# Performance work log

Hardware: AMD Instinct MI355X
Metric: run time of the kernel (lower is better)

## Reference

```python
import jax, jax.numpy as jnp
import numpy as np

NEG_INF = -1e30  # large negative instead of float('-inf') for fp16/bf16 safety in softmax


def setup_inputs() -> dict:
    key = jax.random.key(0)
    k1, k2, k3, k4 = jax.random.split(key, 4)
    B, T, C, H = 8, 2048, 768, 64
    x = jax.random.normal(k1, (B, T, C), dtype=jnp.float32)
    # nn.Linear(n_embd, head_size, bias=False): y = x @ W.T, W shape (head_size, n_embd)
    s = 1.0 / np.sqrt(C)
    Wk = jax.random.uniform(k2, (H, C), dtype=jnp.float32, minval=-s, maxval=s)
    Wq = jax.random.uniform(k3, (H, C), dtype=jnp.float32, minval=-s, maxval=s)
    Wv = jax.random.uniform(k4, (H, C), dtype=jnp.float32, minval=-s, maxval=s)
    return {"x": x, "Wk": Wk, "Wq": Wq, "Wv": Wv}


def reference(x, Wk, Wq, Wv):
    # x: [B,T,C]; Wk/Wq/Wv: [H,C]
    k = jnp.einsum('btc,hc->bth', x, Wk)  # [B,T,H]
    q = jnp.einsum('btc,hc->bth', x, Wq)
    v = jnp.einsum('btc,hc->bth', x, Wv)
    att = jnp.einsum('bqh,bkh->bqk', q, k)  # [B,T,T], NOTE: no 1/sqrt(H) scaling, faithful to source
    T = x.shape[1]
    causal = jnp.tril(jnp.ones((T, T), dtype=bool))
    att = jnp.where(causal, att, NEG_INF)
    att = jax.nn.softmax(att, axis=-1)
    out = jnp.einsum('bqk,bkh->bqh', att, v)  # [B,T,H]
    return out
```

## Files before the change

kernel.cpp:

```cpp
#include <hip/hip_runtime.h>
#include <hip/hip_bf16.h>
#include <stdint.h>

typedef float    f32x4  __attribute__((ext_vector_type(4)));
typedef float    f32x16 __attribute__((ext_vector_type(16)));
typedef short    s16x8  __attribute__((ext_vector_type(8)));
typedef uint32_t u32x4  __attribute__((ext_vector_type(4)));
typedef uint32_t u32x2  __attribute__((ext_vector_type(2)));

#define NB 8
#define NT 2048
#define NC 768
#define NH 64
#define LOG2E 1.4426950408889634f

__device__ __forceinline__ uint32_t f2bf1(float f) {
  union { float f; uint32_t u; } v; v.f = f;
  uint32_t u = v.u;
  return (u + 0x7fffu + ((u >> 16) & 1u)) >> 16;
}
__device__ __forceinline__ uint32_t packbf2(float lo, float hi) {
  union { __hip_bfloat162 h; uint32_t u; } c;
  c.h = __float22bfloat162_rn(float2{lo, hi});
  return c.u;
}
__device__ __forceinline__ float bf2f(short s) {
  union { float f; uint32_t u; } v; v.u = ((uint32_t)(uint16_t)s) << 16; return v.f;
}

__global__ __launch_bounds__(256) void wconv_kernel(
    const float* __restrict__ Wk, const float* __restrict__ Wq,
    const float* __restrict__ Wv, short* __restrict__ Wf)
{
  int f = blockIdx.x * 256 + threadIdx.x;
  int lane = f & 63;
  int rest = f >> 6;
  int ks = rest % 48;
  int nt = rest / 48;
  int col = lane & 31, half = lane >> 5;
  int n = nt * 32 + col;
  int k = ks * 16 + half * 8;
  const float* src;
  float sc = 1.0f;
  if (n < 64)       { src = Wq + (size_t)n * NC + k; sc = LOG2E; }
  else if (n < 128) { src = Wk + (size_t)(n - 64) * NC + k; }
  else              { src = Wv + (size_t)(n - 128) * NC + k; }
  f32x4 a = *(const f32x4*)src;
  f32x4 b = *(const f32x4*)(src + 4);
  u32x4 o = {packbf2(a[0] * sc, a[1] * sc), packbf2(a[2] * sc, a[3] * sc),
             packbf2(b[0] * sc, b[1] * sc), packbf2(b[2] * sc, b[3] * sc)};
  *(u32x4*)&Wf[(size_t)f * 8] = o;
}

__global__ __launch_bounds__(256, 2) void proj_kernel(
    const float* __restrict__ x, const short* __restrict__ Wf,
    short* __restrict__ qf_buf, short* __restrict__ kf_buf, short* __restrict__ vf_buf)
{
  __shared__ char smem[49152];
  short* ldsX  = (short*)smem;
  float* slot0 = (float*)smem;
  float* slot1 = (float*)(smem + 24576);
  short* ldsQT = (short*)(smem + 24576);
  short* ldsKT = ldsQT + 2176;
  short* ldsVT = ldsQT + 4352;

  const int tid  = threadIdx.x;
  const int lane = tid & 63;
  const int w    = tid >> 6;
  const int col  = lane & 31;
  const int half = lane >> 5;
  const int t0   = blockIdx.x * 32;

  {
    const int tok = tid >> 3, g = tid & 7;
    const float* src = x + (size_t)(t0 + tok) * NC + g * 8;
    short* drow = ldsX + tok * 768;
#pragma unroll
    for (int i = 0; i < 12; ++i) {
      f32x4 a = *(const f32x4*)(src + i * 64);
      f32x4 b = *(const f32x4*)(src + i * 64 + 4);
      int grp = g + i * 8;
      int swz = (grp & ~7) | ((grp ^ tok) & 7);
      u32x4 o = {packbf2(a[0], a[1]), packbf2(a[2], a[3]),
                 packbf2(b[0], b[1]), packbf2(b[2], b[3])};
      *(u32x4*)&drow[swz * 8] = o;
    }
  }
  __syncthreads();

  f32x16 acc[6];
#pragma unroll
  for (int j = 0; j < 6; ++j)
#pragma unroll
    for (int e = 0; e < 16; ++e) acc[j][e] = 0.f;

  const short* wbase = Wf + lane * 8;
  auto loadW = [&](s16x8* d, int ks) {
#pragma unroll
    for (int nt = 0; nt < 6; ++nt)
      d[nt] = *(const s16x8*)(wbase + ((size_t)(nt * 48 + ks) << 9));
  };
  auto loadA = [&](int ks) -> s16x8 {
    int grp = ks * 2 + half;
    int swz = (grp & ~7) | ((grp ^ col) & 7);
    return *(const s16x8*)&ldsX[col * 768 + swz * 8];
  };

  {
    const int ks0 = w * 12;
    s16x8 wA[6], wB[6], aA, aB;
    loadW(wA, ks0);
    aA = loadA(ks0);
#pragma unroll
    for (int s = 0; s < 12; s += 2) {
      loadW(wB, ks0 + s + 1);
      aB = loadA(ks0 + s + 1);
#pragma unroll
      for (int nt = 0; nt < 6; ++nt)
        acc[nt] = __builtin_amdgcn_mfma_f32_32x32x16_bf16(aA, wA[nt], acc[nt], 0, 0, 0);
      if (s + 2 < 12) { loadW(wA, ks0 + s + 2); aA = loadA(ks0 + s + 2); }
#pragma unroll
      for (int nt = 0; nt < 6; ++nt)
        acc[nt] = __builtin_amdgcn_mfma_f32_32x32x16_bf16(aB, wB[nt], acc[nt], 0, 0, 0);
    }
  }

  auto putSlot = [&](float* sl) {
#pragma unroll
    for (int nt = 0; nt < 6; ++nt)
#pragma unroll
      for (int r = 0; r < 16; ++r) {
        int rd = (r & 3) + 8 * (r >> 2) + 4 * half;
        sl[rd * 192 + nt * 32 + col] = acc[nt][r];
      }
  };
  auto addSlot = [&](float* sl) {
#pragma unroll
    for (int nt = 0; nt < 6; ++nt)
#pragma unroll
      for (int r = 0; r < 16; ++r) {
        int rd = (r & 3) + 8 * (r >> 2) + 4 * half;
        acc[nt][r] += sl[rd * 192 + nt * 32 + col];
      }
  };

  __syncthreads();
  if (w >= 2) putSlot(w == 2 ? slot0 : slot1);
  __syncthreads();
  if (w < 2) addSlot(w == 0 ? slot0 : slot1);
  __syncthreads();
  if (w == 1) putSlot(slot0);
  __syncthreads();
  if (w == 0) {
    addSlot(slot0);
#pragma unroll
    for (int nt = 0; nt < 6; ++nt) {
      int n = nt * 32 + col;
#pragma unroll
      for (int r = 0; r < 16; ++r) {
        int rd = (r & 3) + 8 * (r >> 2) + 4 * half;
        short v = (short)f2bf1(acc[nt][r]);
        if (n < 64)       ldsQT[rd * 68 + n] = v;
        else if (n < 128) ldsKT[rd * 68 + (n - 64)] = v;
        else              ldsVT[(n - 128) * 34 + rd] = v;
      }
    }
  }
  __syncthreads();

  {
    const int b  = t0 >> 11;
    const int kt = (t0 >> 5) & 63;
    const size_t base = (size_t)(b * 64 + kt) * 2048;
    s16x8 vq = *(const s16x8*)&ldsQT[col * 68 + w * 16 + half * 8];
    *(s16x8*)&qf_buf[base + w * 512 + lane * 8] = vq;
    s16x8 vk = *(const s16x8*)&ldsKT[col * 68 + w * 16 + half * 8];
    *(s16x8*)&kf_buf[base + w * 512 + lane * 8] = vk;
    s16x8 vv = *(const s16x8*)&ldsVT[(col + (w >> 1) * 32) * 34 + (w & 1) * 16 + half * 8];
    *(s16x8*)&vf_buf[base + w * 512 + lane * 8] = vv;
  }
}

__global__ __launch_bounds__(512, 2) void attn_kernel(
    const short* __restrict__ qf_buf, const short* __restrict__ kf_buf,
    const short* __restrict__ vf_buf, float* __restrict__ out)
{
  __shared__ short ldsOb[8][32][72];
  __shared__ float ldsM[8][32];
  __shared__ float ldsL[8][32];

  const int tid  = threadIdx.x;
  const int lane = tid & 63;
  const int w    = tid >> 6;
  const int col  = lane & 31;
  const int half = lane >> 5;
  const int b    = blockIdx.x & 7;
  const int pr   = blockIdx.x >> 3;
  const int qtL = pr, qtH = 63 - pr;
  const int Hn = 64 - pr, Ln = pr + 1;
  int nH = (8 * Hn + 32) / 65;
  if (nH < 1) nH = 1;
  if (nH > 7) nH = 7;
  const int nL = 8 - nH;

  int qt, tBeg, tEnd;
  if (w < nH) { qt = qtH; tBeg = (w * Hn) / nH; tEnd = ((w + 1) * Hn) / nH; }
  else        { int wl = w - nH; qt = qtL; tBeg = (wl * Ln) / nL; tEnd = ((wl + 1) * Ln) / nL; }

  s16x8 qf[4];
  {
    const short* qp = qf_buf + (size_t)(b * 64 + qt) * 2048 + lane * 8;
#pragma unroll
    for (int ks = 0; ks < 4; ++ks) qf[ks] = *(const s16x8*)(qp + ks * 512);
  }
  const short* kfb = kf_buf + (size_t)b * 64 * 2048 + lane * 8;
  const short* vfb = vf_buf + (size_t)b * 64 * 2048 + lane * 8;

  f32x16 oacc[2];
#pragma unroll
  for (int i = 0; i < 2; ++i)
#pragma unroll
    for (int e = 0; e < 16; ++e) oacc[i][e] = 0.f;
  float m = -1e30f, l = 0.f;

  s16x8 kA[4], vA[4], kB[4], vB[4];
  auto loadT = [&](s16x8* dk, s16x8* dv, int t) {
    const short* kp = kfb + (size_t)t * 2048;
    const short* vp = vfb + (size_t)t * 2048;
#pragma unroll
    for (int i = 0; i < 4; ++i) {
      dk[i] = *(const s16x8*)(kp + i * 512);
      dv[i] = *(const s16x8*)(vp + i * 512);
    }
  };
  auto body = [&](s16x8* ck, s16x8* cv, int t) {
    f32x16 s;
#pragma unroll
    for (int e = 0; e < 16; ++e) s[e] = 0.f;
#pragma unroll
    for (int ks = 0; ks < 4; ++ks)
      s = __builtin_amdgcn_mfma_f32_32x32x16_bf16(ck[ks], qf[ks], s, 0, 0, 0);

    if (t == qt) {
#pragma unroll
      for (int r = 0; r < 16; ++r) {
        int rd = (r & 3) + 8 * (r >> 2) + 4 * half;
        if (rd > col) s[r] = -1e30f;
      }
    }
    float vmax = s[0];
#pragma unroll
    for (int r = 1; r < 16; ++r) vmax = fmaxf(vmax, s[r]);
    vmax = fmaxf(vmax, __shfl_xor(vmax, 32));
    float mn    = fmaxf(m, vmax);
    float alpha = exp2f(m - mn);
    float p[16];
    float rs = 0.f;
#pragma unroll
    for (int r = 0; r < 16; ++r) { p[r] = exp2f(s[r] - mn); rs += p[r]; }
    rs += __shfl_xor(rs, 32);
    l = l * alpha + rs;
    m = mn;
#pragma unroll
    for (int i = 0; i < 2; ++i)
#pragma unroll
      for (int e = 0; e < 16; ++e) oacc[i][e] *= alpha;

    uint32_t pw[8];
#pragma unroll
    for (int i = 0; i < 8; ++i) pw[i] = packbf2(p[2 * i], p[2 * i + 1]);
#pragma unroll
    for (int kc = 0; kc < 2; ++kc) {
      uint32_t s0 = half ? pw[4 * kc]     : pw[4 * kc + 2];
      uint32_t s1 = half ? pw[4 * kc + 1] : pw[4 * kc + 3];
      uint32_t r0 = __shfl_xor(s0, 32);
      uint32_t r1 = __shfl_xor(s1, 32);
      uint32_t w0 = half ? r0 : pw[4 * kc];
      uint32_t w1 = half ? r1 : pw[4 * kc + 1];
      uint32_t w2 = half ? pw[4 * kc + 2] : r0;
      uint32_t w3 = half ? pw[4 * kc + 3] : r1;
      union { u32x4 u; s16x8 v; } pf;
      pf.u = (u32x4){w0, w1, w2, w3};
#pragma unroll
      for (int ht = 0; ht < 2; ++ht)
        oacc[ht] = __builtin_amdgcn_mfma_f32_32x32x16_bf16(cv[ht * 2 + kc], pf.v, oacc[ht], 0, 0, 0);
    }
  };

  int t = tBeg;
  if (t < tEnd) loadT(kA, vA, t);
  if (t + 1 < tEnd) loadT(kB, vB, t + 1);
  for (; t + 1 < tEnd; t += 2) {
    body(kA, vA, t);
    if (t + 2 < tEnd) loadT(kA, vA, t + 2);
    body(kB, vB, t + 1);
    if (t + 3 < tEnd) loadT(kB, vB, t + 3);
  }
  if (t < tEnd) body(kA, vA, t);

  if (half == 0) { ldsM[w][col] = m; ldsL[w][col] = l; }
#pragma unroll
  for (int ht = 0; ht < 2; ++ht)
#pragma unroll
    for (int u = 0; u < 4; ++u) {
      int h = ht * 32 + 8 * u + 4 * half;
      u32x2 pk = {packbf2(oacc[ht][4 * u + 0], oacc[ht][4 * u + 1]),
                  packbf2(oacc[ht][4 * u + 2], oacc[ht][4 * u + 3])};
      *(u32x2*)&ldsOb[w][col][h] = pk;
    }
  __syncthreads();

  {
    const int seg = tid >> 8;
    const int rr  = (tid >> 3) & 31;
    const int h0  = (tid & 7) * 8;
    const int s0  = seg ? nH : 0;
    const int s1  = seg ? 8 : nH;
    float M = -1e30f;
    for (int s = s0; s < s1; ++s) M = fmaxf(M, ldsM[s][rr]);
    float Ls = 0.f;
    float o[8];
#pragma unroll
    for (int j = 0; j < 8; ++j) o[j] = 0.f;
    for (int s = s0; s < s1; ++s) {
      float cf = exp2f(ldsM[s][rr] - M);
      Ls += cf * ldsL[s][rr];
      s16x8 raw = *(const s16x8*)&ldsOb[s][rr][h0];
#pragma unroll
      for (int j = 0; j < 8; ++j) o[j] += cf * bf2f(raw[j]);
    }
    float inv = 1.0f / Ls;
    int qrow = (seg ? qtL : qtH) * 32 + rr;
    float* ob = out + (size_t)(b * NT + qrow) * NH + h0;
    *(f32x4*)ob       = (f32x4){o[0] * inv, o[1] * inv, o[2] * inv, o[3] * inv};
    *(f32x4*)(ob + 4) = (f32x4){o[4] * inv, o[5] * inv, o[6] * inv, o[7] * inv};
  }
}

extern "C" void kernel_launch(void* const* d_in, const int* in_sizes, int n_in,
                              void* d_out, int out_size, void* d_ws, size_t ws_size,
                              hipStream_t stream) {
  const float* x  = (const float*)d_in[0];
  const float* Wk = (const float*)d_in[1];
  const float* Wq = (const float*)d_in[2];
  const float* Wv = (const float*)d_in[3];
  float* out = (float*)d_out;

  char* ws = (char*)d_ws;
  short* Wf  = (short*)(ws);
  short* qfb = (short*)(ws + (512 << 10));
  short* kfb = (short*)(ws + (512 << 10) + (2 << 20));
  short* vfb = (short*)(ws + (512 << 10) + (4 << 20));

  hipLaunchKernelGGL(wconv_kernel, dim3(72),  dim3(256), 0, stream, Wk, Wq, Wv, Wf);
  hipLaunchKernelGGL(proj_kernel,  dim3(512), dim3(256), 0, stream, x, Wf, qfb, kfb, vfb);
  hipLaunchKernelGGL(attn_kernel,  dim3(256), dim3(512), 0, stream, qfb, kfb, vfb, out);
}
```

Measured before the change: 115.6 us.

## Fuse projection and attention into one cooperative kernel with grid sync

The projection and attention kernels are merged into a single cooperative launch of 256 blocks of 512 threads. Each block first projects two 32-token tiles, with eight waves splitting K and N four by two, then all blocks meet at a grid-wide barrier before running the attention phase unchanged. This removes one kernel launch and its drain/fill gap. In exchange, the projection phase runs on half as many blocks, the cooperative launch and grid barrier add their own overhead, and correctness depends on all blocks being co-resident.

```diff
diff --git a/kernel.cpp b/kernel.cpp
--- a/kernel.cpp
+++ b/kernel.cpp
@@ -1,6 +1,9 @@
 #include <hip/hip_runtime.h>
 #include <hip/hip_bf16.h>
+#include <hip/hip_cooperative_groups.h>
 #include <stdint.h>
+
+namespace cg = cooperative_groups;
 
 typedef float    f32x4  __attribute__((ext_vector_type(4)));
 typedef float    f32x16 __attribute__((ext_vector_type(16)));
@@ -52,288 +55,294 @@
   *(u32x4*)&Wf[(size_t)f * 8] = o;
 }
 
-__global__ __launch_bounds__(256, 2) void proj_kernel(
+__global__ __launch_bounds__(512, 2) void fused_kernel(
     const float* __restrict__ x, const short* __restrict__ Wf,
-    short* __restrict__ qf_buf, short* __restrict__ kf_buf, short* __restrict__ vf_buf)
+    short* __restrict__ qfb, short* __restrict__ kfb, short* __restrict__ vfb,
+    float* __restrict__ out)
 {
   __shared__ char smem[49152];
-  short* ldsX  = (short*)smem;
-  float* slot0 = (float*)smem;
-  float* slot1 = (float*)(smem + 24576);
-  short* ldsQT = (short*)(smem + 24576);
-  short* ldsKT = ldsQT + 2176;
-  short* ldsVT = ldsQT + 4352;
 
   const int tid  = threadIdx.x;
   const int lane = tid & 63;
-  const int w    = tid >> 6;
+  const int w8   = tid >> 6;
   const int col  = lane & 31;
   const int half = lane >> 5;
-  const int t0   = blockIdx.x * 32;
+  const int blk  = blockIdx.x;
+  const int b    = blk & 7;
+  const int pr   = blk >> 3;
 
   {
-    const int tok = tid >> 3, g = tid & 7;
-    const float* src = x + (size_t)(t0 + tok) * NC + g * 8;
-    short* drow = ldsX + tok * 768;
-#pragma unroll
-    for (int i = 0; i < 12; ++i) {
-      f32x4 a = *(const f32x4*)(src + i * 64);
-      f32x4 b = *(const f32x4*)(src + i * 64 + 4);
-      int grp = g + i * 8;
-      int swz = (grp & ~7) | ((grp ^ tok) & 7);
-      u32x4 o = {packbf2(a[0], a[1]), packbf2(a[2], a[3]),
-                 packbf2(b[0], b[1]), packbf2(b[2], b[3])};
-      *(u32x4*)&drow[swz * 8] = o;
+    short* ldsX = (short*)smem;
+    const int kh = w8 >> 1;
+    const int nh = w8 & 1;
+
+    for (int sub = 0; sub < 2; ++sub) {
+      const int kt = pr * 2 + sub;
+      const int tg = b * 64 + kt;
+      const int t0 = tg * 32;
+
+      {
+        const int tok = tid >> 4, g16 = tid & 15;
+        const float* src = x + (size_t)(t0 + tok) * NC + g16 * 8;
+        short* drow = ldsX + tok * 768;
+#pragma unroll
+        for (int i = 0; i < 6; ++i) {
+          f32x4 a = *(const f32x4*)(src + i * 128);
+          f32x4 c = *(const f32x4*)(src + i * 128 + 4);
+          int grp = g16 + i * 16;
+          int swz = (grp & ~7) | ((grp ^ tok) & 7);
+          u32x4 o = {packbf2(a[0], a[1]), packbf2(a[2], a[3]),
+                     packbf2(c[0], c[1]), packbf2(c[2], c[3])};
+          *(u32x4*)&drow[swz * 8] = o;
+        }
+      }
+      __syncthreads();
+
+      f32x16 acc[3];
+#pragma unroll
+      for (int j = 0; j < 3; ++j)
+#pragma unroll
+        for (int e = 0; e < 16; ++e) acc[j][e] = 0.f;
+
+      const short* wbase = Wf + lane * 8;
+      auto loadW = [&](s16x8* d, int ks) {
+#pragma unroll
+        for (int j = 0; j < 3; ++j)
+          d[j] = *(const s16x8*)(wbase + ((size_t)((nh * 3 + j) * 48 + ks) << 9));
+      };
+      auto loadA = [&](int ks) -> s16x8 {
+        int grp = ks * 2 + half;
+        int swz = (grp & ~7) | ((grp ^ col) & 7);
+        return *(const s16x8*)&ldsX[col * 768 + swz * 8];
+      };
+      {
+        const int ks0 = kh * 12;
+        s16x8 wA[3], wB[3], aA, aB;
+        loadW(wA, ks0); aA = loadA(ks0);
+#pragma unroll
+        for (int s = 0; s < 12; s += 2) {
+          loadW(wB, ks0 + s + 1); aB = loadA(ks0 + s + 1);
+#pragma unroll
+          for (int j = 0; j < 3; ++j)
+            acc[j] = __builtin_amdgcn_mfma_f32_32x32x16_bf16(aA, wA[j], acc[j], 0, 0, 0);
+          if (s + 2 < 12) { loadW(wA, ks0 + s + 2); aA = loadA(ks0 + s + 2); }
+#pragma unroll
+          for (int j = 0; j < 3; ++j)
+            acc[j] = __builtin_amdgcn_mfma_f32_32x32x16_bf16(aB, wB[j], acc[j], 0, 0, 0);
+        }
+      }
+      __syncthreads();
+
+      auto slot = [&](int i) { return (float*)(smem + i * 12288); };
+      auto putSlot = [&](float* sl) {
+#pragma unroll
+        for (int j = 0; j < 3; ++j)
+#pragma unroll
+          for (int r = 0; r < 16; ++r) {
+            int rd = (r & 3) + 8 * (r >> 2) + 4 * half;
+            sl[rd * 96 + j * 32 + col] = acc[j][r];
+          }
+      };
+      auto addSlot = [&](float* sl) {
+#pragma unroll
+        for (int j = 0; j < 3; ++j)
+#pragma unroll
+          for (int r = 0; r < 16; ++r) {
+            int rd = (r & 3) + 8 * (r >> 2) + 4 * half;
+            acc[j][r] += sl[rd * 96 + j * 32 + col];
+          }
+      };
+      if (kh >= 2) putSlot(slot((kh - 2) * 2 + nh));
+      __syncthreads();
+      if (kh == 0) addSlot(slot(nh));
+      if (kh == 1) addSlot(slot(2 + nh));
+      __syncthreads();
+      if (kh == 1) putSlot(slot(nh));
+      __syncthreads();
+
+      short* ldsQT = (short*)(smem + 24576);
+      short* ldsKT = ldsQT + 2176;
+      short* ldsVT = ldsQT + 4352;
+      if (kh == 0) {
+        addSlot(slot(nh));
+#pragma unroll
+        for (int j = 0; j < 3; ++j) {
+          int n = nh * 96 + j * 32 + col;
+#pragma unroll
+          for (int r = 0; r < 16; ++r) {
+            int rd = (r & 3) + 8 * (r >> 2) + 4 * half;
+            short v = (short)f2bf1(acc[j][r]);
+            if (n < 64)       ldsQT[rd * 68 + n] = v;
+            else if (n < 128) ldsKT[rd * 68 + (n - 64)] = v;
+            else              ldsVT[(n - 128) * 34 + rd] = v;
+          }
+        }
+      }
+      __syncthreads();
+
+      {
+        const size_t base = (size_t)tg * 2048;
+        if (w8 < 4) {
+          s16x8 vq = *(const s16x8*)&ldsQT[col * 68 + w8 * 16 + half * 8];
+          *(s16x8*)&qfb[base + w8 * 512 + lane * 8] = vq;
+          s16x8 vk = *(const s16x8*)&ldsKT[col * 68 + w8 * 16 + half * 8];
+          *(s16x8*)&kfb[base + w8 * 512 + lane * 8] = vk;
+        } else {
+          int i = w8 - 4;
+          s16x8 vv = *(const s16x8*)&ldsVT[(col + (i >> 1) * 32) * 34 + (i & 1) * 16 + half * 8];
+          *(s16x8*)&vfb[base + i * 512 + lane * 8] = vv;
+        }
+      }
+      __syncthreads();
     }
   }
-  __syncthreads();
-
-  f32x16 acc[6];
-#pragma unroll
-  for (int j = 0; j < 6; ++j)
-#pragma unroll
-    for (int e = 0; e < 16; ++e) acc[j][e] = 0.f;
-
-  const short* wbase = Wf + lane * 8;
-  auto loadW = [&](s16x8* d, int ks) {
-#pragma unroll
-    for (int nt = 0; nt < 6; ++nt)
-      d[nt] = *(const s16x8*)(wbase + ((size_t)(nt * 48 + ks) << 9));
-  };
-  auto loadA = [&](int ks) -> s16x8 {
-    int grp = ks * 2 + half;
-    int swz = (grp & ~7) | ((grp ^ col) & 7);
-    return *(const s16x8*)&ldsX[col * 768 + swz * 8];
-  };
+
+  cg::this_grid().sync();
 
   {
-    const int ks0 = w * 12;
-    s16x8 wA[6], wB[6], aA, aB;
-    loadW(wA, ks0);
-    aA = loadA(ks0);
-#pragma unroll
-    for (int s = 0; s < 12; s += 2) {
-      loadW(wB, ks0 + s + 1);
-      aB = loadA(ks0 + s + 1);
-#pragma unroll
-      for (int nt = 0; nt < 6; ++nt)
-        acc[nt] = __builtin_amdgcn_mfma_f32_32x32x16_bf16(aA, wA[nt], acc[nt], 0, 0, 0);
-      if (s + 2 < 12) { loadW(wA, ks0 + s + 2); aA = loadA(ks0 + s + 2); }
-#pragma unroll
-      for (int nt = 0; nt < 6; ++nt)
-        acc[nt] = __builtin_amdgcn_mfma_f32_32x32x16_bf16(aB, wB[nt], acc[nt], 0, 0, 0);
+    short* ldsOb = (short*)smem;
+    float* ldsM  = (float*)(smem + 36864);
+    float* ldsL  = (float*)(smem + 37888);
+
+    const int qtL = pr, qtH = 63 - pr;
+    const int Hn = 64 - pr, Ln = pr + 1;
+    int nH = (8 * Hn + 32) / 65;
+    if (nH < 1) nH = 1;
+    if (nH > 7) nH = 7;
+    const int nL = 8 - nH;
+
+    int qt, tBeg, tEnd;
+    if (w8 < nH) { qt = qtH; tBeg = (w8 * Hn) / nH; tEnd = ((w8 + 1) * Hn) / nH; }
+    else         { int wl = w8 - nH; qt = qtL; tBeg = (wl * Ln) / nL; tEnd = ((wl + 1) * Ln) / nL; }
+
+    s16x8 qf[4];
+    {
+      const short* qp = qfb + (size_t)(b * 64 + qt) * 2048 + lane * 8;
+#pragma unroll
+      for (int ks = 0; ks < 4; ++ks) qf[ks] = *(const s16x8*)(qp + ks * 512);
     }
-  }
-
-  auto putSlot = [&](float* sl) {
-#pragma unroll
-    for (int nt = 0; nt < 6; ++nt)
-#pragma unroll
-      for (int r = 0; r < 16; ++r) {
-        int rd = (r & 3) + 8 * (r >> 2) + 4 * half;
-        sl[rd * 192 + nt * 32 + col] = acc[nt][r];
-      }
-  };
-  auto addSlot = [&](float* sl) {
-#pragma unroll
-    for (int nt = 0; nt < 6; ++nt)
-#pragma unroll
-      for (int r = 0; r < 16; ++r) {
-        int rd = (r & 3) + 8 * (r >> 2) + 4 * half;
-        acc[nt][r] += sl[rd * 192 + nt * 32 + col];
-      }
-  };
-
-  __syncthreads();
-  if (w >= 2) putSlot(w == 2 ? slot0 : slot1);
-  __syncthreads();
-  if (w < 2) addSlot(w == 0 ? slot0 : slot1);
-  __syncthreads();
-  if (w == 1) putSlot(slot0);
-  __syncthreads();
-  if (w == 0) {
-    addSlot(slot0);
-#pragma unroll
-    for (int nt = 0; nt < 6; ++nt) {
-      int n = nt * 32 + col;
-#pragma unroll
-      for (int r = 0; r < 16; ++r) {
-        int rd = (r & 3) + 8 * (r >> 2) + 4 * half;
-        short v = (short)f2bf1(acc[nt][r]);
-        if (n < 64)       ldsQT[rd * 68 + n] = v;
-        else if (n < 128) ldsKT[rd * 68 + (n - 64)] = v;
-        else              ldsVT[(n - 128) * 34 + rd] = v;
-      }
+    const short* kfp = kfb + (size_t)b * 64 * 2048 + lane * 8;
+    const short* vfp = vfb + (size_t)b * 64 * 2048 + lane * 8;
+
+    f32x16 oacc[2];
+#pragma unroll
+    for (int i = 0; i < 2; ++i)
+#pragma unroll
+      for (int e = 0; e < 16; ++e) oacc[i][e] = 0.f;
+    float m = -1e30f, l = 0.f;
+
+    s16x8 kA[4], vA[4], kB[4], vB[4];
+    auto loadT = [&](s16x8* dk, s16x8* dv, int t) {
+      const short* kp = kfp + (size_t)t * 2048;
+      const short* vp = vfp + (size_t)t * 2048;
+#pragma unroll
+      for (int i = 0; i < 4; ++i) {
+        dk[i] = *(const s16x8*)(kp + i * 512);
+        dv[i] = *(const s16x8*)(vp + i * 512);
+      }
+    };
+    auto body = [&](s16x8* ck, s16x8* cv, int t) {
+      f32x16 s;
+#pragma unroll
+      for (int e = 0; e < 16; ++e) s[e] = 0.f;
+#pragma unroll
+      for (int ks = 0; ks < 4; ++ks)
+        s = __builtin_amdgcn_mfma_f32_32x32x16_bf16(ck[ks], qf[ks], s, 0, 0, 0);
+
+      if (t == qt) {
+#pragma unroll
+        for (int r = 0; r < 16; ++r) {
+          int rd = (r & 3) + 8 * (r >> 2) + 4 * half;
+          if (rd > col) s[r] = -1e30f;
+        }
+      }
+      float vmax = s[0];
+#pragma unroll
+      for (int r = 1; r < 16; ++r) vmax = fmaxf(vmax, s[r]);
+      vmax = fmaxf(vmax, __shfl_xor(vmax, 32));
+      float mn    = fmaxf(m, vmax);
+      float alpha = exp2f(m - mn);
+      float p[16];
+      float rs = 0.f;
+#pragma unroll
+      for (int r = 0; r < 16; ++r) { p[r] = exp2f(s[r] - mn); rs += p[r]; }
+      rs += __shfl_xor(rs, 32);
+      l = l * alpha + rs;
+      m = mn;
+#pragma unroll
+      for (int i = 0; i < 2; ++i)
+#pragma unroll
+        for (int e = 0; e < 16; ++e) oacc[i][e] *= alpha;
+
+      uint32_t pw[8];
+#pragma unroll
+      for (int i = 0; i < 8; ++i) pw[i] = packbf2(p[2 * i], p[2 * i + 1]);
+#pragma unroll
+      for (int kc = 0; kc < 2; ++kc) {
+        uint32_t s0 = half ? pw[4 * kc]     : pw[4 * kc + 2];
+        uint32_t s1 = half ? pw[4 * kc + 1] : pw[4 * kc + 3];
+        uint32_t r0 = __shfl_xor(s0, 32);
+        uint32_t r1 = __shfl_xor(s1, 32);
+        uint32_t w0 = half ? r0 : pw[4 * kc];
+        uint32_t w1 = half ? r1 : pw[4 * kc + 1];
+        uint32_t w2 = half ? pw[4 * kc + 2] : r0;
+        uint32_t w3 = half ? pw[4 * kc + 3] : r1;
+        union { u32x4 u; s16x8 v; } pf;
+        pf.u = (u32x4){w0, w1, w2, w3};
+#pragma unroll
+        for (int ht = 0; ht < 2; ++ht)
+          oacc[ht] = __builtin_amdgcn_mfma_f32_32x32x16_bf16(cv[ht * 2 + kc], pf.v, oacc[ht], 0, 0, 0);
+      }
+    };
+
+    int t = tBeg;
+    if (t < tEnd) loadT(kA, vA, t);
+    if (t + 1 < tEnd) loadT(kB, vB, t + 1);
+    for (; t + 1 < tEnd; t += 2) {
+      body(kA, vA, t);
+      if (t + 2 < tEnd) loadT(kA, vA, t + 2);
+      body(kB, vB, t + 1);
+      if (t + 3 < tEnd) loadT(kB, vB, t + 3);
     }
-  }
-  __syncthreads();
-
-  {
-    const int b  = t0 >> 11;
-    const int kt = (t0 >> 5) & 63;
-    const size_t base = (size_t)(b * 64 + kt) * 2048;
-    s16x8 vq = *(const s16x8*)&ldsQT[col * 68 + w * 16 + half * 8];
-    *(s16x8*)&qf_buf[base + w * 512 + lane * 8] = vq;
-    s16x8 vk = *(const s16x8*)&ldsKT[col * 68 + w * 16 + half * 8];
-    *(s16x8*)&kf_buf[base + w * 512 + lane * 8] = vk;
-    s16x8 vv = *(const s16x8*)&ldsVT[(col + (w >> 1) * 32) * 34 + (w & 1) * 16 + half * 8];
-    *(s16x8*)&vf_buf[base + w * 512 + lane * 8] = vv;
-  }
-}
-
-__global__ __launch_bounds__(512, 2) void attn_kernel(
-    const short* __restrict__ qf_buf, const short* __restrict__ kf_buf,
-    const short* __restrict__ vf_buf, float* __restrict__ out)
-{
-  __shared__ short ldsOb[8][32][72];
-  __shared__ float ldsM[8][32];
-  __shared__ float ldsL[8][32];
-
-  const int tid  = threadIdx.x;
-  const int lane = tid & 63;
-  const int w    = tid >> 6;
-  const int col  = lane & 31;
-  const int half = lane >> 5;
-  const int b    = blockIdx.x & 7;
-  const int pr   = blockIdx.x >> 3;
-  const int qtL = pr, qtH = 63 - pr;
-  const int Hn = 64 - pr, Ln = pr + 1;
-  int nH = (8 * Hn + 32) / 65;
-  if (nH < 1) nH = 1;
-  if (nH > 7) nH = 7;
-  const int nL = 8 - nH;
-
-  int qt, tBeg, tEnd;
-  if (w < nH) { qt = qtH; tBeg = (w * Hn) / nH; tEnd = ((w + 1) * Hn) / nH; }
-  else        { int wl = w - nH; qt = qtL; tBeg = (wl * Ln) / nL; tEnd = ((wl + 1) * Ln) / nL; }
-
-  s16x8 qf[4];
-  {
-    const short* qp = qf_buf + (size_t)(b * 64 + qt) * 2048 + lane * 8;
-#pragma unroll
-    for (int ks = 0; ks < 4; ++ks) qf[ks] = *(const s16x8*)(qp + ks * 512);
-  }
-  const short* kfb = kf_buf + (size_t)b * 64 * 2048 + lane * 8;
-  const short* vfb = vf_buf + (size_t)b * 64 * 2048 + lane * 8;
-
-  f32x16 oacc[2];
-#pragma unroll
-  for (int i = 0; i < 2; ++i)
-#pragma unroll
-    for (int e = 0; e < 16; ++e) oacc[i][e] = 0.f;
-  float m = -1e30f, l = 0.f;
-
-  s16x8 kA[4], vA[4], kB[4], vB[4];
-  auto loadT = [&](s16x8* dk, s16x8* dv, int t) {
-    const short* kp = kfb + (size_t)t * 2048;
-    const short* vp = vfb + (size_t)t * 2048;
-#pragma unroll
-    for (int i = 0; i < 4; ++i) {
-      dk[i] = *(const s16x8*)(kp + i * 512);
-      dv[i] = *(const s16x8*)(vp + i * 512);
+    if (t < tEnd) body(kA, vA, t);
+
+    if (half == 0) { ldsM[w8 * 32 + col] = m; ldsL[w8 * 32 + col] = l; }
+#pragma unroll
+    for (int ht = 0; ht < 2; ++ht)
+#pragma unroll
+      for (int u = 0; u < 4; ++u) {
+        int h = ht * 32 + 8 * u + 4 * half;
+        u32x2 pk = {packbf2(oacc[ht][4 * u + 0], oacc[ht][4 * u + 1]),
+                    packbf2(oacc[ht][4 * u + 2], oacc[ht][4 * u + 3])};
+        *(u32x2*)&ldsOb[(w8 * 32 + col) * 72 + h] = pk;
+      }
+    __syncthreads();
+
+    {
+      const int seg = tid >> 8;
+      const int rr  = (tid >> 3) & 31;
+      const int h0  = (tid & 7) * 8;
+      const int s0  = seg ? nH : 0;
+      const int s1  = seg ? 8 : nH;
+      float M = -1e30f;
+      for (int s = s0; s < s1; ++s) M = fmaxf(M, ldsM[s * 32 + rr]);
+      float Ls = 0.f;
+      float o[8];
+#pragma unroll
+      for (int j = 0; j < 8; ++j) o[j] = 0.f;
+      for (int s = s0; s < s1; ++s) {
+        float cf = exp2f(ldsM[s * 32 + rr] - M);
+        Ls += cf * ldsL[s * 32 + rr];
+        s16x8 raw = *(const s16x8*)&ldsOb[(s * 32 + rr) * 72 + h0];
+#pragma unroll
+        for (int j = 0; j < 8; ++j) o[j] += cf * bf2f(raw[j]);
+      }
+      float inv = 1.0f / Ls;
+      int qrow = (seg ? qtL : qtH) * 32 + rr;
+      float* ob = out + (size_t)(b * NT + qrow) * NH + h0;
+      *(f32x4*)ob       = (f32x4){o[0] * inv, o[1] * inv, o[2] * inv, o[3] * inv};
+      *(f32x4*)(ob + 4) = (f32x4){o[4] * inv, o[5] * inv, o[6] * inv, o[7] * inv};
     }
-  };
-  auto body = [&](s16x8* ck, s16x8* cv, int t) {
-    f32x16 s;
-#pragma unroll
-    for (int e = 0; e < 16; ++e) s[e] = 0.f;
-#pragma unroll
-    for (int ks = 0; ks < 4; ++ks)
-      s = __builtin_amdgcn_mfma_f32_32x32x16_bf16(ck[ks], qf[ks], s, 0, 0, 0);
-
-    if (t == qt) {
-#pragma unroll
-      for (int r = 0; r < 16; ++r) {
-        int rd = (r & 3) + 8 * (r >> 2) + 4 * half;
-        if (rd > col) s[r] = -1e30f;
-      }
-    }
-    float vmax = s[0];
-#pragma unroll
-    for (int r = 1; r < 16; ++r) vmax = fmaxf(vmax, s[r]);
-    vmax = fmaxf(vmax, __shfl_xor(vmax, 32));
-    float mn    = fmaxf(m, vmax);
-    float alpha = exp2f(m - mn);
-    float p[16];
-    float rs = 0.f;
-#pragma unroll
-    for (int r = 0; r < 16; ++r) { p[r] = exp2f(s[r] - mn); rs += p[r]; }
-    rs += __shfl_xor(rs, 32);
-    l = l * alpha + rs;
-    m = mn;
-#pragma unroll
-    for (int i = 0; i < 2; ++i)
-#pragma unroll
-      for (int e = 0; e < 16; ++e) oacc[i][e] *= alpha;
-
-    uint32_t pw[8];
-#pragma unroll
-    for (int i = 0; i < 8; ++i) pw[i] = packbf2(p[2 * i], p[2 * i + 1]);
-#pragma unroll
-    for (int kc = 0; kc < 2; ++kc) {
-      uint32_t s0 = half ? pw[4 * kc]     : pw[4 * kc + 2];
-      uint32_t s1 = half ? pw[4 * kc + 1] : pw[4 * kc + 3];
-      uint32_t r0 = __shfl_xor(s0, 32);
-      uint32_t r1 = __shfl_xor(s1, 32);
-      uint32_t w0 = half ? r0 : pw[4 * kc];
-      uint32_t w1 = half ? r1 : pw[4 * kc + 1];
-      uint32_t w2 = half ? pw[4 * kc + 2] : r0;
-      uint32_t w3 = half ? pw[4 * kc + 3] : r1;
-      union { u32x4 u; s16x8 v; } pf;
-      pf.u = (u32x4){w0, w1, w2, w3};
-#pragma unroll
-      for (int ht = 0; ht < 2; ++ht)
-        oacc[ht] = __builtin_amdgcn_mfma_f32_32x32x16_bf16(cv[ht * 2 + kc], pf.v, oacc[ht], 0, 0, 0);
-    }
-  };
-
-  int t = tBeg;
-  if (t < tEnd) loadT(kA, vA, t);
-  if (t + 1 < tEnd) loadT(kB, vB, t + 1);
-  for (; t + 1 < tEnd; t += 2) {
-    body(kA, vA, t);
-    if (t + 2 < tEnd) loadT(kA, vA, t + 2);
-    body(kB, vB, t + 1);
-    if (t + 3 < tEnd) loadT(kB, vB, t + 3);
-  }
-  if (t < tEnd) body(kA, vA, t);
-
-  if (half == 0) { ldsM[w][col] = m; ldsL[w][col] = l; }
-#pragma unroll
-  for (int ht = 0; ht < 2; ++ht)
-#pragma unroll
-    for (int u = 0; u < 4; ++u) {
-      int h = ht * 32 + 8 * u + 4 * half;
-      u32x2 pk = {packbf2(oacc[ht][4 * u + 0], oacc[ht][4 * u + 1]),
-                  packbf2(oacc[ht][4 * u + 2], oacc[ht][4 * u + 3])};
-      *(u32x2*)&ldsOb[w][col][h] = pk;
-    }
-  __syncthreads();
-
-  {
-    const int seg = tid >> 8;
-    const int rr  = (tid >> 3) & 31;
-    const int h0  = (tid & 7) * 8;
-    const int s0  = seg ? nH : 0;
-    const int s1  = seg ? 8 : nH;
-    float M = -1e30f;
-    for (int s = s0; s < s1; ++s) M = fmaxf(M, ldsM[s][rr]);
-    float Ls = 0.f;
-    float o[8];
-#pragma unroll
-    for (int j = 0; j < 8; ++j) o[j] = 0.f;
-    for (int s = s0; s < s1; ++s) {
-      float cf = exp2f(ldsM[s][rr] - M);
-      Ls += cf * ldsL[s][rr];
-      s16x8 raw = *(const s16x8*)&ldsOb[s][rr][h0];
-#pragma unroll
-      for (int j = 0; j < 8; ++j) o[j] += cf * bf2f(raw[j]);
-    }
-    float inv = 1.0f / Ls;
-    int qrow = (seg ? qtL : qtH) * 32 + rr;
-    float* ob = out + (size_t)(b * NT + qrow) * NH + h0;
-    *(f32x4*)ob       = (f32x4){o[0] * inv, o[1] * inv, o[2] * inv, o[3] * inv};
-    *(f32x4*)(ob + 4) = (f32x4){o[4] * inv, o[5] * inv, o[6] * inv, o[7] * inv};
   }
 }
 
@@ -352,7 +361,8 @@
   short* kfb = (short*)(ws + (512 << 10) + (2 << 20));
   short* vfb = (short*)(ws + (512 << 10) + (4 << 20));
 
-  hipLaunchKernelGGL(wconv_kernel, dim3(72),  dim3(256), 0, stream, Wk, Wq, Wv, Wf);
-  hipLaunchKernelGGL(proj_kernel,  dim3(512), dim3(256), 0, stream, x, Wf, qfb, kfb, vfb);
-  hipLaunchKernelGGL(attn_kernel,  dim3(256), dim3(512), 0, stream, qfb, kfb, vfb, out);
-}
+  hipLaunchKernelGGL(wconv_kernel, dim3(72), dim3(256), 0, stream, Wk, Wq, Wv, Wf);
+
+  void* args[] = {(void*)&x, (void*)&Wf, (void*)&qfb, (void*)&kfb, (void*)&vfb, (void*)&out};
+  hipLaunchCooperativeKernel((void*)fused_kernel, dim3(256), dim3(512), args, 0, stream);
+}
```

New measurement: 178.4 us. 1.54x slower.
